# Kernel optimization log

Measured on AMD Instinct MI355X. Metric: run time of the kernel, lower is better.

The kernel has to match this reference:

```python
import jax, jax.numpy as jnp
import numpy as np

N_NODES = 100000
N_EDGES = 3200000
IN_CH, HID, OUT_CH = 128, 16, 64


def gcn_conv(x, W, b, row, col, n_nodes):
    # PyG GCNConv: add self loops, symmetric deg^{-1/2} normalization,
    # linear transform, scatter-add aggregation at target nodes (col).
    x = x @ W  # [N, out]
    deg = jax.ops.segment_sum(jnp.ones_like(col, dtype=x.dtype), col,
                              num_segments=n_nodes)  # includes self loops
    inv_sqrt = jnp.where(deg > 0, jax.lax.rsqrt(deg), 0.0)
    norm = inv_sqrt[row] * inv_sqrt[col]  # [E+N]
    msgs = x[row] * norm[:, None]  # gather + scale
    out = jax.ops.segment_sum(msgs, col, num_segments=n_nodes)
    return out + b


def setup_inputs() -> dict:
    key = jax.random.key(0)
    ks = jax.random.split(key, 12)
    x = jax.random.normal(ks[0], (N_NODES, IN_CH), dtype=jnp.float32)
    edge_index = jax.random.randint(ks[1], (2, N_EDGES), 0, N_NODES, dtype=jnp.int64)

    def glorot(k, fan_in, fan_out):
        s = jnp.sqrt(6.0 / (fan_in + fan_out))
        return jax.random.uniform(k, (fan_in, fan_out), jnp.float32, -s, s)

    return {
        'x': x,
        'edge_index': edge_index,
        'conv1_W': glorot(ks[2], IN_CH, HID),
        'conv1_b': jnp.zeros((HID,), jnp.float32),
        'conv2_W': glorot(ks[3], HID, OUT_CH),
        'conv2_b': jnp.zeros((OUT_CH,), jnp.float32),
        't1_W': glorot(ks[4], IN_CH, HID),
        't1_b': jnp.zeros((HID,), jnp.float32),
        't2_W': glorot(ks[5], HID, OUT_CH),
        't2_b': jnp.zeros((OUT_CH,), jnp.float32),
    }


def reference(x, edge_index, conv1_W, conv1_b, conv2_W, conv2_b,
              t1_W, t1_b, t2_W, t2_b):
    n = x.shape[0]
    # add self loops once (fixed shape)
    loops = jnp.arange(n, dtype=edge_index.dtype)
    row = jnp.concatenate([edge_index[0], loops])
    col = jnp.concatenate([edge_index[1], loops])

    identity1 = x @ t1_W + t1_b
    h = jax.nn.relu(gcn_conv(x, conv1_W, conv1_b, row, col, n)) + identity1
    identity2 = h @ t2_W + t2_b
    out = jax.nn.relu(gcn_conv(h, conv2_W, conv2_b, row, col, n)) + identity2
    return out
```

## Files before the change

### kernel.cpp

```cpp
#include <hip/hip_runtime.h>

#define INCH 128
#define C1   16
#define C2   64
#define LOCB 7
#define BNODES (1 << LOCB)
#define CAP  8192
#define ROWBITS 17
#define ROWMASK ((1 << ROWBITS) - 1)
#define SENT 0xFFFFFFFFu
#define ACCP 17
#define FXS   524288.0f
#define INVFX 1.9073486328125e-06f
#define BKT_T 1024
#define AGG_T 512

typedef int iv4 __attribute__((ext_vector_type(4)));
typedef unsigned short usv8 __attribute__((ext_vector_type(8)));

__device__ __forceinline__ unsigned short f2bf(float f) {
    unsigned u = __float_as_uint(f);
    return (unsigned short)((u + 0x7FFF + ((u >> 16) & 1)) >> 16);
}
__device__ __forceinline__ float bf2f(unsigned short s) {
    return __uint_as_float((unsigned)s << 16);
}

__global__ void binit_kernel(int* __restrict__ gcur, int K) {
    int t = blockIdx.x * blockDim.x + threadIdx.x;
    if (t < K) gcur[t] = t * CAP;
}

__global__ __launch_bounds__(BKT_T) void bucket_kernel(
    const int* __restrict__ row, const int* __restrict__ col,
    int* __restrict__ gcur, int* __restrict__ barr,
    int e, int n, int K, int nblocks)
{
    __shared__ int cnt[1024];
    __shared__ int cur[1024];
    __shared__ int sst[1024];
    int tid = threadIdx.x;
    int e4 = e >> 2;
    long b0 = (long)blockIdx.x * e4 / nblocks;
    long b1 = (long)(blockIdx.x + 1) * e4 / nblocks;
    const iv4* c4p = (const iv4*)col;
    const iv4* r4p = (const iv4*)row;
    cnt[tid] = 0;
    __syncthreads();
    for (long i = b0 + tid; i < b1; i += BKT_T) {
        iv4 c4 = c4p[i], r4 = r4p[i];
        #pragma unroll
        for (int k = 0; k < 4; ++k) {
            unsigned c = (unsigned)c4[k], r = (unsigned)r4[k];
            if (c < (unsigned)n && r < (unsigned)n)
                atomicAdd(&cnt[c >> LOCB], 1);
        }
    }
    if (blockIdx.x == 0) {
        for (int i = e4 * 4 + tid; i < e; i += BKT_T) {
            unsigned c = (unsigned)col[i], r = (unsigned)row[i];
            if (c < (unsigned)n && r < (unsigned)n)
                atomicAdd(&cnt[c >> LOCB], 1);
        }
    }
    __syncthreads();
    if (tid < K) {
        int c = cnt[tid];
        int start = c ? atomicAdd(&gcur[tid], (c + 15) & ~15) : 0;
        cur[tid] = start;
        sst[tid] = start;
    }
    __syncthreads();
    for (long i = b0 + tid; i < b1; i += BKT_T) {
        iv4 c4 = c4p[i], r4 = r4p[i];
        #pragma unroll
        for (int k = 0; k < 4; ++k) {
            unsigned c = (unsigned)c4[k], r = (unsigned)r4[k];
            if (c < (unsigned)n && r < (unsigned)n) {
                int b = c >> LOCB;
                int slot = atomicAdd(&cur[b], 1);
                if ((unsigned)slot < (unsigned)((b + 1) * CAP))
                    barr[slot] = (int)(r | ((c & (BNODES - 1)) << ROWBITS));
            }
        }
    }
    if (blockIdx.x == 0) {
        for (int i = e4 * 4 + tid; i < e; i += BKT_T) {
            unsigned c = (unsigned)col[i], r = (unsigned)row[i];
            if (c < (unsigned)n && r < (unsigned)n) {
                int b = c >> LOCB;
                int slot = atomicAdd(&cur[b], 1);
                if ((unsigned)slot < (unsigned)((b + 1) * CAP))
                    barr[slot] = (int)(r | ((c & (BNODES - 1)) << ROWBITS));
            }
        }
    }
    __syncthreads();
    if (tid < K) {
        int c = cnt[tid];
        if (c) {
            int start = sst[tid];
            int end = start + c;
            int re  = start + ((c + 15) & ~15);
            int lim = (tid + 1) * CAP;
            if (end > lim) end = lim;
            if (re  > lim) re  = lim;
            for (int j = end; j < re; ++j) barr[j] = (int)SENT;
        }
    }
}

__global__ __launch_bounds__(AGG_T) void degree_kernel(
    const int* __restrict__ barr, const int* __restrict__ gcur,
    float* __restrict__ inv, int n)
{
    __shared__ int lcnt[BNODES];
    int b = blockIdx.x, tid = threadIdx.x;
    if (tid < BNODES) lcnt[tid] = 0;
    __syncthreads();
    int base = b * CAP;
    int len = gcur[b] - base;
    if (len < 0) len = 0;
    if (len > CAP) len = CAP;
    int len4 = len >> 2;
    const iv4* b4 = (const iv4*)(barr + base);
    for (int i = tid; i < len4; i += AGG_T) {
        iv4 p4 = b4[i];
        #pragma unroll
        for (int k = 0; k < 4; ++k) {
            unsigned pk = (unsigned)p4[k];
            if ((pk & ROWMASK) < (unsigned)n)
                atomicAdd(&lcnt[(pk >> ROWBITS) & (BNODES - 1)], 1);
        }
    }
    __syncthreads();
    if (tid < BNODES) {
        int node = (b << LOCB) + tid;
        if (node < n) inv[node] = rsqrtf((float)lcnt[tid] + 1.0f);
    }
}

__global__ __launch_bounds__(256) void linear1_kernel(
    const float* __restrict__ x, const float* __restrict__ W1,
    const float* __restrict__ T1, const float* __restrict__ t1b,
    const float* __restrict__ inv,
    unsigned short* __restrict__ xW1s_bf, float* __restrict__ xT1, int n)
{
    __shared__ float Wc[INCH][32];
    __shared__ float xs[16][INCH + 4];
    int tid = threadIdx.x;

    for (int i = tid; i < INCH * C1; i += 256) {
        int k = i / C1, c = i % C1;
        Wc[k][c]      = W1[i];
        Wc[k][c + 16] = T1[i];
    }
    int node0 = blockIdx.x * 16;
    for (int i = tid; i < 16 * (INCH / 4); i += 256) {
        int r = i / (INCH / 4);
        int cc = i % (INCH / 4);
        int node = node0 + r;
        float4 v = make_float4(0.f, 0.f, 0.f, 0.f);
        if (node < n) v = ((const float4*)x)[(size_t)node * (INCH / 4) + cc];
        ((float4*)&xs[r][0])[cc] = v;
    }
    __syncthreads();

    int ch = tid & 15, nl = tid >> 4;
    int node = node0 + nl;
    if (node >= n) return;
    float a1 = 0.f, a2 = 0.f;
    #pragma unroll
    for (int k = 0; k < INCH; ++k) {
        float xv = xs[nl][k];
        a1 += xv * Wc[k][ch];
        a2 += xv * Wc[k][ch + 16];
    }
    xW1s_bf[(node << 4) + ch] = f2bf(a1 * inv[node] * FXS);
    xT1[(node << 4) + ch]     = a2 + t1b[ch];
}

#define EDGE_ADDI(PK, V)                                                      \
    do {                                                                      \
        if (((PK) & ROWMASK) < un) {                                          \
            int* _a = &acc[(((PK) >> ROWBITS) & (BNODES - 1))][chb];          \
            _Pragma("unroll")                                                 \
            for (int _j = 0; _j < 8; ++_j)                                    \
                atomicAdd(&_a[_j], (int)rintf(bf2f((V)[_j])));                \
        }                                                                     \
    } while (0)

#define GATHER_SCATTER(SRCBUF)                                                \
    {                                                                         \
        int jj = tid >> 1;                                                    \
        for (int i0 = jj * 4; i0 + 3 < len; i0 += (AGG_T * 2)) {              \
            iv4 w = *(const iv4*)(bp + i0);                                   \
            unsigned s0 = (unsigned)w[0] & ROWMASK, s1 = (unsigned)w[1] & ROWMASK; \
            unsigned s2 = (unsigned)w[2] & ROWMASK, s3 = (unsigned)w[3] & ROWMASK; \
            unsigned c0 = s0 < un ? s0 : 0u, c1 = s1 < un ? s1 : 0u;          \
            unsigned c2 = s2 < un ? s2 : 0u, c3 = s3 < un ? s3 : 0u;          \
            usv8 v0 = *(const usv8*)(SRCBUF + ((size_t)c0 << 4) + chb);       \
            usv8 v1 = *(const usv8*)(SRCBUF + ((size_t)c1 << 4) + chb);       \
            usv8 v2 = *(const usv8*)(SRCBUF + ((size_t)c2 << 4) + chb);       \
            usv8 v3 = *(const usv8*)(SRCBUF + ((size_t)c3 << 4) + chb);       \
            EDGE_ADDI((unsigned)w[0], v0);                                    \
            EDGE_ADDI((unsigned)w[1], v1);                                    \
            EDGE_ADDI((unsigned)w[2], v2);                                    \
            EDGE_ADDI((unsigned)w[3], v3);                                    \
        }                                                                     \
    }

__global__ __launch_bounds__(AGG_T) void agg1_bucket_kernel(
    const int* __restrict__ barr, const int* __restrict__ gcur,
    const float* __restrict__ inv, const unsigned short* __restrict__ xW1s_bf,
    const float* __restrict__ xT1, const float* __restrict__ b1,
    float* __restrict__ h, unsigned short* __restrict__ hs_bf, int n)
{
    __shared__ int acc[BNODES][ACCP];
    int b = blockIdx.x, tid = threadIdx.x;
    for (int i = tid; i < BNODES * ACCP; i += AGG_T) (&acc[0][0])[i] = 0;
    __syncthreads();

    int base = b * CAP;
    int len = gcur[b] - base;
    if (len < 0) len = 0;
    if (len > CAP) len = CAP;
    const int* bp = barr + base;
    unsigned un = (unsigned)n;
    int chb = (tid & 1) << 3;

    GATHER_SCATTER(xW1s_bf)
    __syncthreads();

    for (int t = tid; t < BNODES * C1; t += AGG_T) {
        int loc = t >> 4, ch = t & 15;
        int node = (b << LOCB) + loc;
        if (node >= n) continue;
        int idx = (node << 4) + ch;
        float ic = inv[node];
        float v = ((float)acc[loc][ch] + bf2f(xW1s_bf[idx])) * INVFX * ic + b1[ch];
        float hv = fmaxf(v, 0.f) + xT1[idx];
        h[idx]     = hv;
        hs_bf[idx] = f2bf(hv * ic * FXS);
    }
}

__global__ __launch_bounds__(AGG_T) void agg2_bucket_kernel(
    const int* __restrict__ barr, const int* __restrict__ gcur,
    const float* __restrict__ inv, const unsigned short* __restrict__ hs_bf,
    const float* __restrict__ h,
    const float* __restrict__ W2, const float* __restrict__ T2,
    const float* __restrict__ b2, const float* __restrict__ t2b,
    float* __restrict__ out, int n)
{
    __shared__ int   acc[BNODES][ACCP];
    __shared__ float Wc[C1][128];
    __shared__ float h_s[BNODES][C1];
    float* accf = (float*)&acc[0][0];
    int b = blockIdx.x, tid = threadIdx.x;
    for (int i = tid; i < BNODES * ACCP; i += AGG_T) (&acc[0][0])[i] = 0;
    for (int i = tid; i < C1 * 128; i += AGG_T) {
        int k = i >> 7, c = i & 127;
        Wc[k][c] = (c < 64) ? W2[k * C2 + c] : T2[k * C2 + (c - 64)];
    }
    {
        int node0 = b << LOCB;
        for (int t = tid; t < BNODES * C1 / 4; t += AGG_T) {
            float4 v = make_float4(0.f, 0.f, 0.f, 0.f);
            if (node0 + (t >> 2) < n) v = ((const float4*)h)[(size_t)node0 * 4 + t];
            ((float4*)&h_s[0][0])[t] = v;
        }
    }
    __syncthreads();

    int base = b * CAP;
    int len = gcur[b] - base;
    if (len < 0) len = 0;
    if (len > CAP) len = CAP;
    const int* bp = barr + base;
    unsigned un = (unsigned)n;
    int chb = (tid & 1) << 3;

    GATHER_SCATTER(hs_bf)
    __syncthreads();

    for (int t = tid; t < BNODES * C1; t += AGG_T) {
        int loc = t >> 4, ch = t & 15;
        int node = (b << LOCB) + loc;
        float v = 0.f;
        if (node < n)
            v = ((float)acc[loc][ch] + bf2f(hs_bf[(node << 4) + ch])) * INVFX * inv[node];
        accf[loc * ACCP + ch] = v;
    }
    __syncthreads();

    int och = tid & 63, g = tid >> 6;
    float w1r[C1], w2r[C1];
    #pragma unroll
    for (int k = 0; k < C1; ++k) { w1r[k] = Wc[k][och]; w2r[k] = Wc[k][och + 64]; }
    float bb = b2[och], tb = t2b[och];
    for (int q = 0; q < 16; ++q) {
        int loc = (g << 4) + q;
        int node2 = (b << LOCB) + loc;
        if (node2 >= n) continue;
        float s1 = bb, s2 = tb;
        #pragma unroll
        for (int k = 0; k < C1; ++k) {
            s1 += accf[loc * ACCP + k] * w1r[k];
            s2 += h_s[loc][k]          * w2r[k];
        }
        out[(size_t)node2 * C2 + och] = fmaxf(s1, 0.f) + s2;
    }
}

extern "C" void kernel_launch(void* const* d_in, const int* in_sizes, int n_in,
                              void* d_out, int out_size, void* d_ws, size_t ws_size,
                              hipStream_t stream) {
    const float* x   = (const float*)d_in[0];
    const int*   ei  = (const int*)d_in[1];
    const float* W1  = (const float*)d_in[2];
    const float* b1  = (const float*)d_in[3];
    const float* W2  = (const float*)d_in[4];
    const float* b2  = (const float*)d_in[5];
    const float* T1  = (const float*)d_in[6];
    const float* t1b = (const float*)d_in[7];
    const float* T2  = (const float*)d_in[8];
    const float* t2b = (const float*)d_in[9];
    float* out = (float*)d_out;

    const int n = in_sizes[0] / INCH;
    const int e = in_sizes[1] / 2;
    const int* row = ei;
    const int* col = ei + e;
    const int K = (n + BNODES - 1) >> LOCB;

    char* ws = (char*)d_ws;
    int*   gcur  = (int*)ws;                          ws += 4096;
    float* inv   = (float*)ws;                        ws += (size_t)n * 4;
    float* xT1   = (float*)ws;                        ws += (size_t)n * C1 * 4;
    float* h     = (float*)ws;                        ws += (size_t)n * C1 * 4;
    unsigned short* xW1s_bf = (unsigned short*)ws;    ws += (size_t)n * C1 * 2;
    unsigned short* hs_bf   = (unsigned short*)ws;    ws += (size_t)n * C1 * 2;
    int*   barr  = (int*)ws;                          ws += (size_t)K * CAP * 4;

    const int nbb = 390;

    binit_kernel  <<<(K + 255) / 256, 256, 0, stream>>>(gcur, K);
    bucket_kernel <<<nbb, BKT_T, 0, stream>>>(row, col, gcur, barr, e, n, K, nbb);
    degree_kernel <<<K, AGG_T, 0, stream>>>(barr, gcur, inv, n);

    linear1_kernel <<<(n + 15) / 16, 256, 0, stream>>>(x, W1, T1, t1b, inv, xW1s_bf, xT1, n);
    agg1_bucket_kernel<<<K, AGG_T, 0, stream>>>(barr, gcur, inv, xW1s_bf, xT1, b1, h, hs_bf, n);
    agg2_bucket_kernel<<<K, AGG_T, 0, stream>>>(barr, gcur, inv, hs_bf, h,
                                                W2, T2, b2, t2b, out, n);
}
```

Before: 251.8 us.

## Pack two biased fixed-point channels per 64-bit LDS atomic in aggregation

Lowers the fixed-point scale and packs two channels into one 64-bit shared-memory atomicAdd. Each value is stored with a bias so it stays a non-negative 32-bit lane, and the bias times the node degree is subtracted afterwards. This halves the number of LDS atomics per edge in both aggregation kernels. It adds a deg array and a smaller scale, so there is less precision and some risk of carry or overflow between lanes for high-degree nodes.

```diff
diff --git a/kernel.cpp b/kernel.cpp
--- a/kernel.cpp
+++ b/kernel.cpp
@@ -9,9 +9,11 @@
 #define ROWBITS 17
 #define ROWMASK ((1 << ROWBITS) - 1)
 #define SENT 0xFFFFFFFFu
-#define ACCP 17
-#define FXS   524288.0f
-#define INVFX 1.9073486328125e-06f
+#define ACC2P 9
+#define FXS   16384.0f
+#define INVFX 6.103515625e-05f
+#define FXBH  524288.5f
+#define BSH   19
 #define BKT_T 1024
 #define AGG_T 512
 
@@ -112,7 +114,7 @@
 
 __global__ __launch_bounds__(AGG_T) void degree_kernel(
     const int* __restrict__ barr, const int* __restrict__ gcur,
-    float* __restrict__ inv, int n)
+    float* __restrict__ inv, int* __restrict__ deg, int n)
 {
     __shared__ int lcnt[BNODES];
     int b = blockIdx.x, tid = threadIdx.x;
@@ -136,7 +138,10 @@
     __syncthreads();
     if (tid < BNODES) {
         int node = (b << LOCB) + tid;
-        if (node < n) inv[node] = rsqrtf((float)lcnt[tid] + 1.0f);
+        if (node < n) {
+            deg[node] = lcnt[tid];
+            inv[node] = rsqrtf((float)lcnt[tid] + 1.0f);
+        }
     }
 }
 
@@ -180,13 +185,16 @@
     xT1[(node << 4) + ch]     = a2 + t1b[ch];
 }
 
-#define EDGE_ADDI(PK, V)                                                      \
+#define EDGE_ADDI64(PK, V)                                                    \
     do {                                                                      \
         if (((PK) & ROWMASK) < un) {                                          \
-            int* _a = &acc[(((PK) >> ROWBITS) & (BNODES - 1))][chb];          \
+            unsigned long long* _a = &acc[(((PK) >> ROWBITS) & (BNODES - 1))][tb]; \
             _Pragma("unroll")                                                 \
-            for (int _j = 0; _j < 8; ++_j)                                    \
-                atomicAdd(&_a[_j], (int)rintf(bf2f((V)[_j])));                \
+            for (int _j = 0; _j < 4; ++_j) {                                  \
+                unsigned _lo = (unsigned)(bf2f((V)[2 * _j])     + FXBH);      \
+                unsigned _hi = (unsigned)(bf2f((V)[2 * _j + 1]) + FXBH);      \
+                atomicAdd(&_a[_j], ((unsigned long long)_hi << 32) | _lo);    \
+            }                                                                 \
         }                                                                     \
     } while (0)
 
@@ -203,22 +211,23 @@
             usv8 v1 = *(const usv8*)(SRCBUF + ((size_t)c1 << 4) + chb);       \
             usv8 v2 = *(const usv8*)(SRCBUF + ((size_t)c2 << 4) + chb);       \
             usv8 v3 = *(const usv8*)(SRCBUF + ((size_t)c3 << 4) + chb);       \
-            EDGE_ADDI((unsigned)w[0], v0);                                    \
-            EDGE_ADDI((unsigned)w[1], v1);                                    \
-            EDGE_ADDI((unsigned)w[2], v2);                                    \
-            EDGE_ADDI((unsigned)w[3], v3);                                    \
+            EDGE_ADDI64((unsigned)w[0], v0);                                  \
+            EDGE_ADDI64((unsigned)w[1], v1);                                  \
+            EDGE_ADDI64((unsigned)w[2], v2);                                  \
+            EDGE_ADDI64((unsigned)w[3], v3);                                  \
         }                                                                     \
     }
 
 __global__ __launch_bounds__(AGG_T) void agg1_bucket_kernel(
     const int* __restrict__ barr, const int* __restrict__ gcur,
-    const float* __restrict__ inv, const unsigned short* __restrict__ xW1s_bf,
+    const float* __restrict__ inv, const int* __restrict__ deg,
+    const unsigned short* __restrict__ xW1s_bf,
     const float* __restrict__ xT1, const float* __restrict__ b1,
     float* __restrict__ h, unsigned short* __restrict__ hs_bf, int n)
 {
-    __shared__ int acc[BNODES][ACCP];
+    __shared__ unsigned long long acc[BNODES][ACC2P];
     int b = blockIdx.x, tid = threadIdx.x;
-    for (int i = tid; i < BNODES * ACCP; i += AGG_T) (&acc[0][0])[i] = 0;
+    for (int i = tid; i < BNODES * ACC2P; i += AGG_T) (&acc[0][0])[i] = 0ull;
     __syncthreads();
 
     int base = b * CAP;
@@ -228,6 +237,7 @@
     const int* bp = barr + base;
     unsigned un = (unsigned)n;
     int chb = (tid & 1) << 3;
+    int tb  = (tid & 1) << 2;
 
     GATHER_SCATTER(xW1s_bf)
     __syncthreads();
@@ -237,8 +247,11 @@
         int node = (b << LOCB) + loc;
         if (node >= n) continue;
         int idx = (node << 4) + ch;
+        unsigned long long w = acc[loc][ch >> 1];
+        unsigned wd = (ch & 1) ? (unsigned)(w >> 32) : (unsigned)w;
+        int sv = (int)(wd - ((unsigned)deg[node] << BSH));
         float ic = inv[node];
-        float v = ((float)acc[loc][ch] + bf2f(xW1s_bf[idx])) * INVFX * ic + b1[ch];
+        float v = ((float)sv + bf2f(xW1s_bf[idx])) * INVFX * ic + b1[ch];
         float hv = fmaxf(v, 0.f) + xT1[idx];
         h[idx]     = hv;
         hs_bf[idx] = f2bf(hv * ic * FXS);
@@ -247,18 +260,18 @@
 
 __global__ __launch_bounds__(AGG_T) void agg2_bucket_kernel(
     const int* __restrict__ barr, const int* __restrict__ gcur,
-    const float* __restrict__ inv, const unsigned short* __restrict__ hs_bf,
-    const float* __restrict__ h,
+    const float* __restrict__ inv, const int* __restrict__ deg,
+    const unsigned short* __restrict__ hs_bf, const float* __restrict__ h,
     const float* __restrict__ W2, const float* __restrict__ T2,
     const float* __restrict__ b2, const float* __restrict__ t2b,
     float* __restrict__ out, int n)
 {
-    __shared__ int   acc[BNODES][ACCP];
+    __shared__ unsigned long long acc[BNODES][ACC2P];
     __shared__ float Wc[C1][128];
     __shared__ float h_s[BNODES][C1];
-    float* accf = (float*)&acc[0][0];
+    __shared__ float accf[BNODES][C1 + 1];
     int b = blockIdx.x, tid = threadIdx.x;
-    for (int i = tid; i < BNODES * ACCP; i += AGG_T) (&acc[0][0])[i] = 0;
+    for (int i = tid; i < BNODES * ACC2P; i += AGG_T) (&acc[0][0])[i] = 0ull;
     for (int i = tid; i < C1 * 128; i += AGG_T) {
         int k = i >> 7, c = i & 127;
         Wc[k][c] = (c < 64) ? W2[k * C2 + c] : T2[k * C2 + (c - 64)];
@@ -280,6 +293,7 @@
     const int* bp = barr + base;
     unsigned un = (unsigned)n;
     int chb = (tid & 1) << 3;
+    int tb  = (tid & 1) << 2;
 
     GATHER_SCATTER(hs_bf)
     __syncthreads();
@@ -288,9 +302,13 @@
         int loc = t >> 4, ch = t & 15;
         int node = (b << LOCB) + loc;
         float v = 0.f;
-        if (node < n)
-            v = ((float)acc[loc][ch] + bf2f(hs_bf[(node << 4) + ch])) * INVFX * inv[node];
-        accf[loc * ACCP + ch] = v;
+        if (node < n) {
+            unsigned long long w = acc[loc][ch >> 1];
+            unsigned wd = (ch & 1) ? (unsigned)(w >> 32) : (unsigned)w;
+            int sv = (int)(wd - ((unsigned)deg[node] << BSH));
+            v = ((float)sv + bf2f(hs_bf[(node << 4) + ch])) * INVFX * inv[node];
+        }
+        accf[loc][ch] = v;
     }
     __syncthreads();
 
@@ -298,16 +316,16 @@
     float w1r[C1], w2r[C1];
     #pragma unroll
     for (int k = 0; k < C1; ++k) { w1r[k] = Wc[k][och]; w2r[k] = Wc[k][och + 64]; }
-    float bb = b2[och], tb = t2b[och];
+    float bb = b2[och], tb2 = t2b[och];
     for (int q = 0; q < 16; ++q) {
         int loc = (g << 4) + q;
         int node2 = (b << LOCB) + loc;
         if (node2 >= n) continue;
-        float s1 = bb, s2 = tb;
+        float s1 = bb, s2 = tb2;
         #pragma unroll
         for (int k = 0; k < C1; ++k) {
-            s1 += accf[loc * ACCP + k] * w1r[k];
-            s2 += h_s[loc][k]          * w2r[k];
+            s1 += accf[loc][k] * w1r[k];
+            s2 += h_s[loc][k]  * w2r[k];
         }
         out[(size_t)node2 * C2 + och] = fmaxf(s1, 0.f) + s2;
     }
@@ -337,6 +355,7 @@
     char* ws = (char*)d_ws;
     int*   gcur  = (int*)ws;                          ws += 4096;
     float* inv   = (float*)ws;                        ws += (size_t)n * 4;
+    int*   deg   = (int*)ws;                          ws += (size_t)n * 4;
     float* xT1   = (float*)ws;                        ws += (size_t)n * C1 * 4;
     float* h     = (float*)ws;                        ws += (size_t)n * C1 * 4;
     unsigned short* xW1s_bf = (unsigned short*)ws;    ws += (size_t)n * C1 * 2;
@@ -347,10 +366,10 @@
 
     binit_kernel  <<<(K + 255) / 256, 256, 0, stream>>>(gcur, K);
     bucket_kernel <<<nbb, BKT_T, 0, stream>>>(row, col, gcur, barr, e, n, K, nbb);
-    degree_kernel <<<K, AGG_T, 0, stream>>>(barr, gcur, inv, n);
+    degree_kernel <<<K, AGG_T, 0, stream>>>(barr, gcur, inv, deg, n);
 
     linear1_kernel <<<(n + 15) / 16, 256, 0, stream>>>(x, W1, T1, t1b, inv, xW1s_bf, xT1, n);
-    agg1_bucket_kernel<<<K, AGG_T, 0, stream>>>(barr, gcur, inv, xW1s_bf, xT1, b1, h, hs_bf, n);
-    agg2_bucket_kernel<<<K, AGG_T, 0, stream>>>(barr, gcur, inv, hs_bf, h,
+    agg1_bucket_kernel<<<K, AGG_T, 0, stream>>>(barr, gcur, inv, deg, xW1s_bf, xT1, b1, h, hs_bf, n);
+    agg2_bucket_kernel<<<K, AGG_T, 0, stream>>>(barr, gcur, inv, deg, hs_bf, h,
                                                 W2, T2, b2, t2b, out, n);
 }
```

Result: no change. 249.6 us (-0.9%).
